# Performance work log

Hardware: AMD Instinct MI355X
Metric: run time of the kernel (lower is better)

## Reference

```python
import jax, jax.numpy as jnp
import numpy as np
from jax import lax

IN_CH = 64
PROTO = 20
CLS = 4
B, H, Wd, D = 2, 64, 64, 64


def setup_inputs() -> dict:
    key = jax.random.key(0)
    ks = jax.random.split(key, 9)
    return {
        "x": jax.random.normal(ks[0], (B, IN_CH, H, Wd, D), dtype=jnp.float32),
        "w_to": jax.random.normal(ks[1], (CLS, IN_CH), dtype=jnp.float32) * 0.1,
        "b_to": jax.random.normal(ks[2], (CLS,), dtype=jnp.float32) * 0.1,
        "w_from": jax.random.normal(ks[3], (IN_CH, CLS), dtype=jnp.float32) * 0.1,
        "b_from": jax.random.normal(ks[4], (IN_CH,), dtype=jnp.float32) * 0.1,
        "W": jax.random.normal(ks[5], (PROTO, CLS), dtype=jnp.float32),
        "BETA": jax.random.normal(ks[6], (PROTO, CLS), dtype=jnp.float32) * 0.5,
        "alpha": jnp.zeros((PROTO, 1), dtype=jnp.float32),
        "gamma": jnp.full((PROTO, 1), 0.1, dtype=jnp.float32),
    }


def reference(x, w_to, b_to, w_from, b_from, W, BETA, alpha, gamma):
    # 1x1x1 conv to evidence space: [B,4,H,W,D]
    ev = jnp.einsum('bchwd,oc->bohwd', x, w_to) + b_to[None, :, None, None, None]

    BETA2 = BETA * BETA                                   # [P,4]
    U = BETA2 / BETA2.sum(1, keepdims=True)               # [P,4] membership degrees
    alphap = 0.99 / (1.0 + jnp.exp(-alpha[:, 0]))         # [P]
    g2 = gamma[:, 0] ** 2                                 # [P]

    dt = ev.dtype
    bshape = (ev.shape[0],) + ev.shape[2:]                # [B,H,W,D]

    def step(mk, per_proto):
        Wk, Uk, ap_k, g2_k = per_proto
        # RBF activation for prototype k
        diff = ev - Wk[None, :, None, None, None]          # [B,4,H,W,D]
        d = 0.5 * jnp.sum(diff * diff, axis=1)            # [B,H,W,D]
        s = ap_k * jnp.exp(-g2_k * d)                     # [B,H,W,D]
        m_c = Uk[:, None, None, None, None] * s[None]      # [4,B,H,W,D]
        m5 = 1.0 - s                                       # [B,H,W,D]
        # Dempster's rule of combination (unnormalized)
        mk_c, mk5 = mk[:CLS], mk[CLS]
        new_c = mk_c * (m_c + m5[None]) + m_c * mk5[None]
        new5 = mk5 * m5
        return jnp.concatenate([new_c, new5[None]], axis=0), None

    mk0 = jnp.concatenate(
        [jnp.zeros((CLS,) + bshape, dtype=dt), jnp.ones((1,) + bshape, dtype=dt)], axis=0)
    mk, _ = lax.scan(step, mk0, (W, U, alphap, g2))        # [5,B,H,W,D]

    K = mk.sum(0)                                          # [B,H,W,D]
    mk_n = jnp.transpose(mk / K[None], (1, 0, 2, 3, 4))    # [B,5,H,W,D]

    # add ignorance mass to each class, map back to feature space
    evid = mk_n[:, :CLS] + mk_n[:, CLS:CLS + 1]            # [B,4,H,W,D]
    out = jnp.einsum('bchwd,oc->bohwd', evid, w_from) + b_from[None, :, None, None, None]
    return out
```

## Files before the change

### kernel.cpp

```cpp
#include <hip/hip_runtime.h>


constexpr int kInCh    = 64;
constexpr int kCls     = 4;
constexpr int kProto   = 20;
constexpr long kSpatial = 64L * 64L * 64L;
constexpr int kVec     = 4;
constexpr int kChunk   = 16;

typedef float f32x4 __attribute__((ext_vector_type(4)));

__global__ __launch_bounds__(256, 4) void evi_fused_kernel(
    const float* __restrict__ x,
    const float* __restrict__ w_to,
    const float* __restrict__ b_to,
    const float* __restrict__ w_from,
    const float* __restrict__ b_from,
    const float* __restrict__ Wm,
    const float* __restrict__ BETA,
    const float* __restrict__ alpha,
    const float* __restrict__ gamma,
    float* __restrict__ out)
{
    __shared__ float s_wt[kCls * kInCh];
    __shared__ float s_wf[kInCh * kCls];
    __shared__ float s_bf[kInCh];
    __shared__ float s_bto[kCls];
    __shared__ float s_W[kProto][kCls];
    __shared__ float s_U[kProto][kCls];
    __shared__ float s_ap[kProto];
    __shared__ float s_g2[kProto];

    const int t = threadIdx.x;

    s_wt[t] = w_to[t];
    s_wf[t] = w_from[t];
    if (t < kInCh) s_bf[t] = b_from[t];
    if (t < kCls)  s_bto[t] = b_to[t];
    if (t < kProto) {
        float bsq[kCls];
        float sum = 0.f;
        #pragma unroll
        for (int c = 0; c < kCls; ++c) {
            const float bb = BETA[t * kCls + c];
            bsq[c] = bb * bb;
            sum += bsq[c];
        }
        const float inv = 1.0f / sum;
        #pragma unroll
        for (int c = 0; c < kCls; ++c) {
            s_U[t][c] = bsq[c] * inv;
            s_W[t][c] = Wm[t * kCls + c];
        }
        s_ap[t] = 0.99f / (1.0f + expf(-alpha[t]));
        const float g = gamma[t];
        s_g2[t] = g * g;
    }
    __syncthreads();

    const int tid   = blockIdx.x * blockDim.x + t;
    const int wave  = tid >> 6;
    const int lane  = tid & 63;
    const int chunk = lane >> 4;
    const int vg    = wave * 16 + (lane & 15);

    const int vgPerBatch = (int)(kSpatial / kVec);
    const int b = vg >> 16;
    const int r = vg & (vgPerBatch - 1);
    const size_t base = (size_t)b * kInCh * kSpatial + (size_t)r * kVec;
    const int c0 = chunk * kChunk;

    float ev[kCls][kVec];
    #pragma unroll
    for (int o = 0; o < kCls; ++o)
        #pragma unroll
        for (int v = 0; v < kVec; ++v) ev[o][v] = 0.0f;

    #pragma unroll
    for (int j = 0; j < kChunk; ++j) {
        const int c = c0 + j;
        const f32x4 xv = *reinterpret_cast<const f32x4*>(x + base + (size_t)c * kSpatial);
        #pragma unroll
        for (int o = 0; o < kCls; ++o) {
            const float w = s_wt[o * kInCh + c];
            ev[o][0] += xv.x * w;
            ev[o][1] += xv.y * w;
            ev[o][2] += xv.z * w;
            ev[o][3] += xv.w * w;
        }
    }

    #pragma unroll
    for (int o = 0; o < kCls; ++o)
        #pragma unroll
        for (int v = 0; v < kVec; ++v) {
            float e = ev[o][v];
            e += __shfl_xor(e, 16, 64);
            e += __shfl_xor(e, 32, 64);
            ev[o][v] = e + s_bto[o];
        }

    float mkc[kCls][kVec];
    float mk5[kVec];
    #pragma unroll
    for (int v = 0; v < kVec; ++v) {
        mk5[v] = 1.0f;
        #pragma unroll
        for (int c = 0; c < kCls; ++c) mkc[c][v] = 0.0f;
    }

    for (int k = 0; k < kProto; ++k) {
        float Wk[kCls], Uk[kCls];
        #pragma unroll
        for (int c = 0; c < kCls; ++c) { Wk[c] = s_W[k][c]; Uk[c] = s_U[k][c]; }
        const float ap = s_ap[k];
        const float g2 = s_g2[k];
        #pragma unroll
        for (int v = 0; v < kVec; ++v) {
            float d = 0.0f;
            #pragma unroll
            for (int c = 0; c < kCls; ++c) {
                const float df = ev[c][v] - Wk[c];
                d += df * df;
            }
            d *= 0.5f;
            const float s  = ap * __expf(-g2 * d);
            const float m5 = 1.0f - s;
            const float old5 = mk5[v];
            #pragma unroll
            for (int c = 0; c < kCls; ++c) {
                const float mc = Uk[c] * s;
                mkc[c][v] = mkc[c][v] * (mc + m5) + mc * old5;
            }
            mk5[v] = old5 * m5;
        }
    }

    #pragma unroll
    for (int v = 0; v < kVec; ++v) {
        float K = mk5[v];
        #pragma unroll
        for (int c = 0; c < kCls; ++c) K += mkc[c][v];
        const float inv = 1.0f / K;
        #pragma unroll
        for (int c = 0; c < kCls; ++c) mkc[c][v] = (mkc[c][v] + mk5[v]) * inv;
    }

    #pragma unroll
    for (int j = 0; j < kChunk; ++j) {
        const int o = c0 + j;
        const float w0 = s_wf[o * kCls + 0];
        const float w1 = s_wf[o * kCls + 1];
        const float w2 = s_wf[o * kCls + 2];
        const float w3 = s_wf[o * kCls + 3];
        const float bo = s_bf[o];
        f32x4 acc;
        acc.x = bo + mkc[0][0]*w0 + mkc[1][0]*w1 + mkc[2][0]*w2 + mkc[3][0]*w3;
        acc.y = bo + mkc[0][1]*w0 + mkc[1][1]*w1 + mkc[2][1]*w2 + mkc[3][1]*w3;
        acc.z = bo + mkc[0][2]*w0 + mkc[1][2]*w1 + mkc[2][2]*w2 + mkc[3][2]*w3;
        acc.w = bo + mkc[0][3]*w0 + mkc[1][3]*w1 + mkc[2][3]*w2 + mkc[3][3]*w3;
        __builtin_nontemporal_store(acc, reinterpret_cast<f32x4*>(out + base + (size_t)o * kSpatial));
    }
}

extern "C" void kernel_launch(void* const* d_in, const int* in_sizes, int n_in,
                              void* d_out, int out_size, void* d_ws, size_t ws_size,
                              hipStream_t stream) {
    const float* x      = (const float*)d_in[0];
    const float* w_to   = (const float*)d_in[1];
    const float* b_to   = (const float*)d_in[2];
    const float* w_from = (const float*)d_in[3];
    const float* b_from = (const float*)d_in[4];
    const float* Wm     = (const float*)d_in[5];
    const float* BETA   = (const float*)d_in[6];
    const float* alpha  = (const float*)d_in[7];
    const float* gamma  = (const float*)d_in[8];
    float* out = (float*)d_out;

    const int block = 256;
    const int grid  = 2048;
    evi_fused_kernel<<<grid, block, 0, stream>>>(x, w_to, b_to, w_from, b_from,
                                                 Wm, BETA, alpha, gamma, out);
}
```

Before: 52.05 us.

## Assign one thread per voxel group across all channels, dropping cross-lane reduction

Each thread now handles all 64 input channels for its 4 voxels, loading 16 channels at a time before computing. This removes the shuffle reduction and the fourfold redundant prototype computation per voxel group. The grid shrinks from 2048 to 512 blocks and the launch-bounds occupancy hint is removed. The trade-off is fewer waves in flight and more registers per thread, which may reduce memory-latency hiding.

```diff
diff --git a/kernel.cpp b/kernel.cpp
--- a/kernel.cpp
+++ b/kernel.cpp
@@ -6,11 +6,12 @@
 constexpr int kProto   = 20;
 constexpr long kSpatial = 64L * 64L * 64L;
 constexpr int kVec     = 4;
-constexpr int kChunk   = 16;
+constexpr int kGrpPerBatch = (int)(kSpatial / kVec);
+constexpr int kBatch   = 16;
 
 typedef float f32x4 __attribute__((ext_vector_type(4)));
 
-__global__ __launch_bounds__(256, 4) void evi_fused_kernel(
+__global__ __launch_bounds__(256) void evi_fused_kernel(
     const float* __restrict__ x,
     const float* __restrict__ w_to,
     const float* __restrict__ b_to,
@@ -58,47 +59,39 @@
     }
     __syncthreads();
 
-    const int tid   = blockIdx.x * blockDim.x + t;
-    const int wave  = tid >> 6;
-    const int lane  = tid & 63;
-    const int chunk = lane >> 4;
-    const int vg    = wave * 16 + (lane & 15);
-
-    const int vgPerBatch = (int)(kSpatial / kVec);
-    const int b = vg >> 16;
-    const int r = vg & (vgPerBatch - 1);
+    const int tid = blockIdx.x * blockDim.x + t;
+    const int b   = tid >> 16;
+    const int r   = tid & (kGrpPerBatch - 1);
     const size_t base = (size_t)b * kInCh * kSpatial + (size_t)r * kVec;
-    const int c0 = chunk * kChunk;
 
     float ev[kCls][kVec];
     #pragma unroll
     for (int o = 0; o < kCls; ++o)
         #pragma unroll
-        for (int v = 0; v < kVec; ++v) ev[o][v] = 0.0f;
+        for (int v = 0; v < kVec; ++v) ev[o][v] = s_bto[o];
 
     #pragma unroll
-    for (int j = 0; j < kChunk; ++j) {
-        const int c = c0 + j;
-        const f32x4 xv = *reinterpret_cast<const f32x4*>(x + base + (size_t)c * kSpatial);
+    for (int bb = 0; bb < kInCh / kBatch; ++bb) {
+        const int cb = bb * kBatch;
+        f32x4 xv[kBatch];
         #pragma unroll
-        for (int o = 0; o < kCls; ++o) {
-            const float w = s_wt[o * kInCh + c];
-            ev[o][0] += xv.x * w;
-            ev[o][1] += xv.y * w;
-            ev[o][2] += xv.z * w;
-            ev[o][3] += xv.w * w;
+        for (int j = 0; j < kBatch; ++j)
+            xv[j] = *reinterpret_cast<const f32x4*>(x + base + (size_t)(cb + j) * kSpatial);
+        __builtin_amdgcn_sched_barrier(0);
+
+        #pragma unroll
+        for (int j = 0; j < kBatch; ++j) {
+            const int c = cb + j;
+            #pragma unroll
+            for (int o = 0; o < kCls; ++o) {
+                const float w = s_wt[o * kInCh + c];
+                ev[o][0] += xv[j].x * w;
+                ev[o][1] += xv[j].y * w;
+                ev[o][2] += xv[j].z * w;
+                ev[o][3] += xv[j].w * w;
+            }
         }
     }
-
-    #pragma unroll
-    for (int o = 0; o < kCls; ++o)
-        #pragma unroll
-        for (int v = 0; v < kVec; ++v) {
-            float e = ev[o][v];
-            e += __shfl_xor(e, 16, 64);
-            e += __shfl_xor(e, 32, 64);
-            ev[o][v] = e + s_bto[o];
-        }
 
     float mkc[kCls][kVec];
     float mk5[kVec];
@@ -110,11 +103,11 @@
     }
 
     for (int k = 0; k < kProto; ++k) {
+        const float ap = s_ap[k];
+        const float g2 = s_g2[k];
         float Wk[kCls], Uk[kCls];
         #pragma unroll
         for (int c = 0; c < kCls; ++c) { Wk[c] = s_W[k][c]; Uk[c] = s_U[k][c]; }
-        const float ap = s_ap[k];
-        const float g2 = s_g2[k];
         #pragma unroll
         for (int v = 0; v < kVec; ++v) {
             float d = 0.0f;
@@ -136,6 +129,7 @@
         }
     }
 
+    float evid[kCls][kVec];
     #pragma unroll
     for (int v = 0; v < kVec; ++v) {
         float K = mk5[v];
@@ -143,22 +137,21 @@
         for (int c = 0; c < kCls; ++c) K += mkc[c][v];
         const float inv = 1.0f / K;
         #pragma unroll
-        for (int c = 0; c < kCls; ++c) mkc[c][v] = (mkc[c][v] + mk5[v]) * inv;
+        for (int c = 0; c < kCls; ++c) evid[c][v] = (mkc[c][v] + mk5[v]) * inv;
     }
 
     #pragma unroll
-    for (int j = 0; j < kChunk; ++j) {
-        const int o = c0 + j;
+    for (int o = 0; o < kInCh; ++o) {
         const float w0 = s_wf[o * kCls + 0];
         const float w1 = s_wf[o * kCls + 1];
         const float w2 = s_wf[o * kCls + 2];
         const float w3 = s_wf[o * kCls + 3];
         const float bo = s_bf[o];
         f32x4 acc;
-        acc.x = bo + mkc[0][0]*w0 + mkc[1][0]*w1 + mkc[2][0]*w2 + mkc[3][0]*w3;
-        acc.y = bo + mkc[0][1]*w0 + mkc[1][1]*w1 + mkc[2][1]*w2 + mkc[3][1]*w3;
-        acc.z = bo + mkc[0][2]*w0 + mkc[1][2]*w1 + mkc[2][2]*w2 + mkc[3][2]*w3;
-        acc.w = bo + mkc[0][3]*w0 + mkc[1][3]*w1 + mkc[2][3]*w2 + mkc[3][3]*w3;
+        acc.x = bo + evid[0][0]*w0 + evid[1][0]*w1 + evid[2][0]*w2 + evid[3][0]*w3;
+        acc.y = bo + evid[0][1]*w0 + evid[1][1]*w1 + evid[2][1]*w2 + evid[3][1]*w3;
+        acc.z = bo + evid[0][2]*w0 + evid[1][2]*w1 + evid[2][2]*w2 + evid[3][2]*w3;
+        acc.w = bo + evid[0][3]*w0 + evid[1][3]*w1 + evid[2][3]*w2 + evid[3][3]*w3;
         __builtin_nontemporal_store(acc, reinterpret_cast<f32x4*>(out + base + (size_t)o * kSpatial));
     }
 }
@@ -178,7 +171,7 @@
     float* out = (float*)d_out;
 
     const int block = 256;
-    const int grid  = 2048;
+    const int grid  = 512;
     evi_fused_kernel<<<grid, block, 0, stream>>>(x, w_to, b_to, w_from, b_from,
                                                  Wm, BETA, alpha, gamma, out);
 }
```

Result: faster. 49.88 us (-4.2%).
